# Kernel tuning notes

Hardware: AMD Instinct MI355X
Metric: run time of the kernel (lower is better)

## Reference

```python
import jax, jax.numpy as jnp
import numpy as np

B, N, C, H, P = 8, 4096, 512, 8, 64
D = C // H


def setup_inputs() -> dict:
    key = jax.random.key(0)
    ks = jax.random.split(key, 5)
    s = 0.02
    return {
        "x": jax.random.normal(ks[0], (B, N, C), jnp.float32),
        "w_qkv": jax.random.normal(ks[1], (3 * C, C), jnp.float32) * s,
        "w_e": jax.random.normal(ks[2], (P, N), jnp.float32) * s,
        "b_e": jnp.zeros((P,), jnp.float32),
        "temperature": jnp.ones((1, 1, 1), jnp.float32),
        "temperature2": jnp.ones((H, 1, 1), jnp.float32),
        "w_o1": jax.random.normal(ks[3], (C // 2, C), jnp.float32) * s,
        "b_o1": jnp.zeros((C // 2,), jnp.float32),
        "w_o2": jax.random.normal(ks[4], (C // 2, C), jnp.float32) * s,
        "b_o2": jnp.zeros((C // 2,), jnp.float32),
    }


def reference(x, w_qkv, w_e, b_e, temperature, temperature2, w_o1, b_o1, w_o2, b_o2):
    Bs, Ns, Cs = x.shape
    # qkvv projection and head split: [B,N,3C] -> [3,B,H,N,D]
    qkv = (x @ w_qkv.T).reshape(Bs, Ns, 3, H, D)
    qkv = jnp.transpose(qkv, (2, 0, 3, 1, 4))
    q, k, v = qkv[0], qkv[1], qkv[2]
    q_t = jnp.swapaxes(q, -2, -1)  # [B,H,D,N]
    k_t = jnp.swapaxes(k, -2, -1)  # [B,H,D,N]
    v_t = jnp.swapaxes(v, -2, -1)  # [B,H,D,N]
    # Linformer-style projection along token axis; E = F (shared weights)
    kp = k_t @ w_e.T + b_e  # [B,H,D,P]
    vp = v_t @ w_e.T + b_e  # [B,H,D,P]
    # L2-normalize q along tokens (k is normalized in the original AFTER
    # projection, so that normalization is dead code and omitted)
    qn = q_t / jnp.maximum(jnp.linalg.norm(q_t, axis=-1, keepdims=True), 1e-12)
    # ---- channel attention: [B,C,C] scores over raw x ----
    xt = jnp.swapaxes(x, -2, -1)  # [B,C,N]
    attn_ca = jax.nn.softmax((xt @ x) * temperature, axis=-1)
    x_ca = jnp.swapaxes(attn_ca @ xt, -2, -1)  # [B,N,C]
    # ---- projected spatial attention: [B,H,N,P] scores ----
    attn_sa = jax.nn.softmax(
        jnp.einsum('bhdn,bhdp->bhnp', qn, kp) * temperature2, axis=-1)
    x_sa = jnp.einsum('bhnp,bhdp->bhnd', attn_sa, vp)  # [B,H,N,D]
    # faithful to torch: permute(0,3,1,2) then reshape(B,N,C)
    x_sa = jnp.transpose(x_sa, (0, 3, 1, 2)).reshape(Bs, Ns, Cs)
    out = jnp.concatenate(
        [x_sa @ w_o1.T + b_o1, x_ca @ w_o2.T + b_o2], axis=-1)
    return out
```

## Files before the change

### kernel.cpp

```cpp
#include <hip/hip_runtime.h>
#include <hip/hip_bf16.h>

typedef unsigned short u16;

#define AS1 __attribute__((address_space(1)))
#define AS3 __attribute__((address_space(3)))

static __device__ __forceinline__ float bl(u16 v) {
    return __uint_as_float(((unsigned)v) << 16);
}
static __device__ __forceinline__ u16 f2b(float f) {
    unsigned u = __float_as_uint(f);
    unsigned r = u + 0x7FFFu + ((u >> 16) & 1u);
    return (u16)(r >> 16);
}
static __device__ __forceinline__ float ldf(const void* p, long i, int isbf) {
    if (isbf) return bl(((const u16*)p)[i]);
    return ((const float*)p)[i];
}
static __device__ __forceinline__ void gload_lds16(const u16* g, u16* l) {
    __builtin_amdgcn_global_load_lds((const AS1 void*)g, (AS3 void*)l, 16, 0, 0);
}

typedef __attribute__((ext_vector_type(8))) short bf16x8;
typedef __attribute__((ext_vector_type(4))) float f32x4;

static __device__ __forceinline__ bf16x8 pack8(const float* p) {
    const float4 x0 = ((const float4*)p)[0];
    const float4 x1 = ((const float4*)p)[1];
    unsigned r0, r1, r2, r3;
    asm("v_cvt_pk_bf16_f32 %0, %1, %2" : "=v"(r0) : "v"(x0.x), "v"(x0.y));
    asm("v_cvt_pk_bf16_f32 %0, %1, %2" : "=v"(r1) : "v"(x0.z), "v"(x0.w));
    asm("v_cvt_pk_bf16_f32 %0, %1, %2" : "=v"(r2) : "v"(x1.x), "v"(x1.y));
    asm("v_cvt_pk_bf16_f32 %0, %1, %2" : "=v"(r3) : "v"(x1.z), "v"(x1.w));
    union { unsigned u[4]; bf16x8 v; } u;
    u.u[0] = r0; u.u[1] = r1; u.u[2] = r2; u.u[3] = r3;
    return u.v;
}

__global__ void dtype_probe(const void* __restrict__ temp, unsigned* __restrict__ flag) {
    if (threadIdx.x == 0 && blockIdx.x == 0)
        flag[0] = (((const u16*)temp)[0] == 0x3F80) ? 1u : 0u;
}

__global__ __launch_bounds__(256) void zero_f32(float* __restrict__ p, long n) {
    const long stride = (long)gridDim.x * 256;
    for (long i = (long)blockIdx.x * 256 + threadIdx.x; i < n; i += stride)
        p[i] = 0.f;
}

__global__ __launch_bounds__(256) void conv_x(const void* __restrict__ X,
                                              u16* __restrict__ xb,
                                              u16* __restrict__ xt,
                                              const unsigned* __restrict__ flg)
{
    __shared__ u16 tile[64][65];
    const int f = (int)flg[0];
    const int b = blockIdx.z;
    const int n0 = blockIdx.x * 64, c0 = blockIdx.y * 64;
    const int t = threadIdx.x, r0 = t >> 6, c = t & 63;
    #pragma unroll
    for (int rr = 0; rr < 16; ++rr) {
        const int r = rr * 4 + r0;
        const long gi = ((long)b * 4096 + n0 + r) * 512 + c0 + c;
        const u16 h = f2b(ldf(X, gi, f));
        xb[gi] = h;
        tile[r][c] = h;
    }
    __syncthreads();
    #pragma unroll
    for (int rr = 0; rr < 16; ++rr) {
        const int cc = rr * 4 + r0;
        xt[((long)b * 512 + c0 + cc) * 4096 + n0 + c] = tile[c][cc];
    }
}

__global__ __launch_bounds__(256) void conv_w(const void* __restrict__ W,
                                              u16* __restrict__ wb, long nelem,
                                              const unsigned* __restrict__ flg)
{
    const int f = (int)flg[0];
    const long stride = (long)gridDim.x * 256;
    for (long i = (long)blockIdx.x * 256 + threadIdx.x; i < nelem; i += stride)
        wb[i] = f2b(ldf(W, i, f));
}

__global__ __launch_bounds__(512, 2) void gemm256_nt(
    const u16* __restrict__ A, const u16* __restrict__ B,
    void* __restrict__ C, const void* __restrict__ bias,
    int K, int lda, int ldb, int ldc,
    long sA, long sB, long sC,
    const unsigned* __restrict__ flg, int biasExt, int cF32,
    float* __restrict__ qsq,
    const u16* __restrict__ A2, const u16* __restrict__ B2,
    const void* __restrict__ bias2, int nSwitch)
{
    __shared__ u16 Asm[2][256 * 32];
    __shared__ u16 Bsm[2][256 * 32];
    const int t = threadIdx.x, w = t >> 6, l = t & 63;
    const int gx = gridDim.x, gy = gridDim.y;
    const long nwg = (long)gx * gy * gridDim.z;
    const long lin = blockIdx.x + (long)gx * (blockIdx.y + (long)gy * blockIdx.z);
    long nid = lin;
    if ((nwg & 7) == 0) nid = (lin & 7) * (nwg >> 3) + (lin >> 3);
    const int by = (int)(nid % gy);
    const long r2 = nid / gy;
    const int bx = (int)(r2 % gx);
    const int bz = (int)(r2 / gx);
    const int m0 = bx * 256, n0 = by * 256;
    const u16* Asel = A; const u16* Bsel = B; const void* bsel = bias;
    int nLoc = n0;
    if (A2 && n0 >= nSwitch) { Asel = A2; Bsel = B2; bsel = bias2; nLoc = n0 - nSwitch; }
    const u16* Ab = Asel + (long)bz * sA;
    const u16* Bb = Bsel + (long)bz * sB + (long)nLoc * ldb;
    const int wm = (w >> 1) * 64, wn = (w & 1) * 128;
    const int srow = l >> 2;
    const int selem = (((l & 3) ^ (srow & 3)) << 3);
    const int fr = l & 15;
    const int fk = (l >> 4) * 8;
    const int xorv = (fr & 3) << 3;
    f32x4 acc[4][8];
    #pragma unroll
    for (int i = 0; i < 4; ++i)
        #pragma unroll
        for (int j = 0; j < 8; ++j)
            acc[i][j] = (f32x4){0.f, 0.f, 0.f, 0.f};

#define STAGE256(nb, kk)                                                                     \
    do {                                                                                     \
        gload_lds16(Ab + (long)(m0 + w * 16 + srow) * lda + (kk) + selem, &Asm[nb][w * 512]);        \
        gload_lds16(Ab + (long)(m0 + (w + 8) * 16 + srow) * lda + (kk) + selem, &Asm[nb][(w + 8) * 512]); \
        gload_lds16(Bb + (long)(w * 16 + srow) * ldb + (kk) + selem, &Bsm[nb][w * 512]);             \
        gload_lds16(Bb + (long)((w + 8) * 16 + srow) * ldb + (kk) + selem, &Bsm[nb][(w + 8) * 512]);     \
    } while (0)

    STAGE256(0, 0);
    __syncthreads();
    int cur = 0;
    for (int k0 = 0; k0 < K; k0 += 32) {
        if (k0 + 32 < K) STAGE256(cur ^ 1, k0 + 32);
        bf16x8 af[4], bf[8];
        #pragma unroll
        for (int i = 0; i < 4; ++i)
            af[i] = *(const bf16x8*)&Asm[cur][((wm + i * 16 + fr) << 5) + (fk ^ xorv)];
        #pragma unroll
        for (int j = 0; j < 8; ++j)
            bf[j] = *(const bf16x8*)&Bsm[cur][((wn + j * 16 + fr) << 5) + (fk ^ xorv)];
        #pragma unroll
        for (int i = 0; i < 4; ++i)
            #pragma unroll
            for (int j = 0; j < 8; ++j)
                acc[i][j] = __builtin_amdgcn_mfma_f32_16x16x32_bf16(af[i], bf[j], acc[i][j], 0, 0, 0);
        __syncthreads();
        cur ^= 1;
    }
#undef STAGE256

    const int f = (int)flg[0];
    const long cOff = (long)bz * sC;
    float bj[8];
    #pragma unroll
    for (int j = 0; j < 8; ++j) bj[j] = 0.f;
    if (bsel) {
        #pragma unroll
        for (int j = 0; j < 8; ++j)
            bj[j] = ldf(bsel, (nLoc & 255) + wn + j * 16 + fr, biasExt ? f : 1);
    }
    #pragma unroll
    for (int i = 0; i < 4; ++i) {
        #pragma unroll
        for (int j = 0; j < 8; ++j) {
            const int col = n0 + wn + j * 16 + fr;
            #pragma unroll
            for (int r = 0; r < 4; ++r) {
                const int row = m0 + wm + i * 16 + (l >> 4) * 4 + r;
                const float v = acc[i][j][r] + bj[j];
                if (cF32) ((float*)C)[cOff + (long)row * ldc + col] = v;
                else      ((u16*)C)[cOff + (long)row * ldc + col] = f2b(v);
            }
        }
    }
    if (qsq) {
        #pragma unroll
        for (int j = 0; j < 8; ++j) {
            const int col = n0 + wn + j * 16 + fr;
            if (col < 512) {
                float s = 0.f;
                #pragma unroll
                for (int i = 0; i < 4; ++i)
                    #pragma unroll
                    for (int r = 0; r < 4; ++r)
                        s = fmaf(acc[i][j][r], acc[i][j][r], s);
                s += __shfl_xor(s, 16, 64);
                s += __shfl_xor(s, 32, 64);
                if ((l >> 4) == 0)
                    atomicAdd(&qsq[(long)bz * 512 + col], s);
            }
        }
    }
}

__global__ __launch_bounds__(512, 2) void gram256_sym(
    const u16* __restrict__ XT, float* __restrict__ S)
{
    __shared__ u16 Asm[2][256 * 32];
    __shared__ u16 Bsm[2][256 * 32];
    const int t = threadIdx.x, w = t >> 6, l = t & 63;
    const int tx = blockIdx.x, b = blockIdx.y, kz = blockIdx.z;
    const int diag = (tx != 1);
    const int m0 = (tx == 2) ? 256 : 0;
    const int n0 = (tx == 0) ? 0 : 256;
    const u16* Ab = XT + (long)b * 512 * 4096 + (long)m0 * 4096;
    const u16* Bb = XT + (long)b * 512 * 4096 + (long)n0 * 4096;
    const int wm = (w >> 1) * 64, wn = (w & 1) * 128;
    const int srow = l >> 2;
    const int selem = (((l & 3) ^ (srow & 3)) << 3);
    const int fr = l & 15;
    const int fk = (l >> 4) * 8;
    const int xorv = (fr & 3) << 3;
    f32x4 acc[4][8];
    #pragma unroll
    for (int i = 0; i < 4; ++i)
        #pragma unroll
        for (int j = 0; j < 8; ++j)
            acc[i][j] = (f32x4){0.f, 0.f, 0.f, 0.f};

#define GSTAGE(nb, kk)                                                                       \
    do {                                                                                     \
        gload_lds16(Ab + (long)(w * 16 + srow) * 4096 + (kk) + selem, &Asm[nb][w * 512]);            \
        gload_lds16(Ab + (long)((w + 8) * 16 + srow) * 4096 + (kk) + selem, &Asm[nb][(w + 8) * 512]);    \
        if (!diag) {                                                                         \
            gload_lds16(Bb + (long)(w * 16 + srow) * 4096 + (kk) + selem, &Bsm[nb][w * 512]);        \
            gload_lds16(Bb + (long)((w + 8) * 16 + srow) * 4096 + (kk) + selem, &Bsm[nb][(w + 8) * 512]); \
        }                                                                                    \
    } while (0)

    const int kBeg = kz * 1024, kEnd = kBeg + 1024;
    GSTAGE(0, kBeg);
    __syncthreads();
    int cur = 0;
    for (int k0 = kBeg; k0 < kEnd; k0 += 32) {
        if (k0 + 32 < kEnd) GSTAGE(cur ^ 1, k0 + 32);
        const u16* Bsrc = diag ? &Asm[cur][0] : &Bsm[cur][0];
        bf16x8 af[4], bf[8];
        #pragma unroll
        for (int i = 0; i < 4; ++i)
            af[i] = *(const bf16x8*)&Asm[cur][((wm + i * 16 + fr) << 5) + (fk ^ xorv)];
        #pragma unroll
        for (int j = 0; j < 8; ++j)
            bf[j] = *(const bf16x8*)&Bsrc[((wn + j * 16 + fr) << 5) + (fk ^ xorv)];
        #pragma unroll
        for (int i = 0; i < 4; ++i)
            #pragma unroll
            for (int j = 0; j < 8; ++j)
                acc[i][j] = __builtin_amdgcn_mfma_f32_16x16x32_bf16(af[i], bf[j], acc[i][j], 0, 0, 0);
        __syncthreads();
        cur ^= 1;
    }
#undef GSTAGE

    float* Sb = S + (long)b * 262144;
    #pragma unroll
    for (int i = 0; i < 4; ++i) {
        #pragma unroll
        for (int j = 0; j < 8; ++j) {
            const int col = n0 + wn + j * 16 + fr;
            #pragma unroll
            for (int r = 0; r < 4; ++r) {
                const int row = m0 + wm + i * 16 + (l >> 4) * 4 + r;
                const float v = acc[i][j][r];
                atomicAdd(&Sb[(long)row * 512 + col], v);
                if (!diag) atomicAdd(&Sb[(long)col * 512 + row], v);
            }
        }
    }
}

__global__ __launch_bounds__(256) void xe_mfma(const u16* __restrict__ WEB,
                                               const u16* __restrict__ XT,
                                               float* __restrict__ XE)
{
    const int t = threadIdx.x, w = t >> 6, l = t & 63;
    const int l15 = l & 15, g = l >> 4;
    const int c0 = blockIdx.x * 128 + (w >> 1) * 64;
    const int b = blockIdx.y;
    const int nbase = blockIdx.z * 512 + (w & 1) * 256;
    f32x4 acc[4][4];
    #pragma unroll
    for (int i = 0; i < 4; ++i)
        #pragma unroll
        for (int j = 0; j < 4; ++j)
            acc[i][j] = (f32x4){0.f, 0.f, 0.f, 0.f};
    for (int ks = 0; ks < 8; ++ks) {
        const int n = nbase + ks * 32 + g * 8;
        bf16x8 a[4], bb[4];
        #pragma unroll
        for (int i = 0; i < 4; ++i)
            a[i] = *(const bf16x8*)&WEB[(long)(i * 16 + l15) * 4096 + n];
        #pragma unroll
        for (int j = 0; j < 4; ++j)
            bb[j] = *(const bf16x8*)&XT[((long)b * 512 + c0 + j * 16 + l15) * 4096 + n];
        #pragma unroll
        for (int i = 0; i < 4; ++i)
            #pragma unroll
            for (int j = 0; j < 4; ++j)
                acc[i][j] = __builtin_amdgcn_mfma_f32_16x16x32_bf16(a[i], bb[j], acc[i][j], 0, 0, 0);
    }
    #pragma unroll
    for (int i = 0; i < 4; ++i)
        #pragma unroll
        for (int j = 0; j < 4; ++j)
            #pragma unroll
            for (int r = 0; r < 4; ++r)
                atomicAdd(&XE[((long)b * 64 + i * 16 + g * 4 + r) * 512 + c0 + j * 16 + l15],
                          acc[i][j][r]);
}

__global__ __launch_bounds__(256) void kpvp2_mfma(const float* __restrict__ XE,
                                                  const u16* __restrict__ WQB,
                                                  const float* __restrict__ qsq,
                                                  const void* __restrict__ be,
                                                  const void* __restrict__ temp2,
                                                  u16* __restrict__ kpT,
                                                  u16* __restrict__ vpB,
                                                  const unsigned* __restrict__ flg)
{
    __shared__ float lds[4][4096];
    const int bh = blockIdx.x, b = bh >> 3, h = bh & 7;
    const int t = threadIdx.x, w = t >> 6, l = t & 63;
    const int l15 = l & 15, g = l >> 4;
    const int isV = w >> 1;
    const int ch = w & 1;
    const u16* wrow = WQB + (long)(512 + isV * 512 + h * 64) * 512;
    const float* xr = XE + (long)b * 64 * 512;
    f32x4 acc[4][4];
    #pragma unroll
    for (int i = 0; i < 4; ++i)
        #pragma unroll
        for (int j = 0; j < 4; ++j)
            acc[i][j] = (f32x4){0.f, 0.f, 0.f, 0.f};
    for (int ks = 0; ks < 8; ++ks) {
        const int c = ch * 256 + ks * 32 + g * 8;
        bf16x8 a[4], bb[4];
        if (!isV) {
            #pragma unroll
            for (int i = 0; i < 4; ++i)
                a[i] = pack8(&xr[(long)(i * 16 + l15) * 512 + c]);
            #pragma unroll
            for (int j = 0; j < 4; ++j)
                bb[j] = *(const bf16x8*)&wrow[(long)(j * 16 + l15) * 512 + c];
        } else {
            #pragma unroll
            for (int i = 0; i < 4; ++i)
                a[i] = *(const bf16x8*)&wrow[(long)(i * 16 + l15) * 512 + c];
            #pragma unroll
            for (int j = 0; j < 4; ++j)
                bb[j] = pack8(&xr[(long)(j * 16 + l15) * 512 + c]);
        }
        #pragma unroll
        for (int i = 0; i < 4; ++i)
            #pragma unroll
            for (int j = 0; j < 4; ++j)
                acc[i][j] = __builtin_amdgcn_mfma_f32_16x16x32_bf16(a[i], bb[j], acc[i][j], 0, 0, 0);
    }
    #pragma unroll
    for (int i = 0; i < 4; ++i)
        #pragma unroll
        for (int j = 0; j < 4; ++j)
            #pragma unroll
            for (int r = 0; r < 4; ++r)
                lds[w][(i * 16 + g * 4 + r) * 64 + j * 16 + l15] = acc[i][j][r];
    __syncthreads();
    const int f = (int)flg[0];
    if (t < 128) {
        const float t2 = ldf(temp2, h, f);
        for (int e = t; e < 4096; e += 128) {
            const int p = e >> 6, d = e & 63;
            const float rn = 1.0f / fmaxf(sqrtf(qsq[b * 512 + h * 64 + d]), 1e-12f);
            kpT[(long)bh * 4096 + e] = f2b((lds[0][e] + lds[1][e] + ldf(be, p, f)) * rn * t2);
        }
    } else {
        for (int e = t - 128; e < 4096; e += 128) {
            vpB[(long)bh * 4096 + e] = f2b(lds[2][e] + lds[3][e] + ldf(be, e & 63, f));
        }
    }
}

__global__ __launch_bounds__(256) void softmax_ca(const float* __restrict__ S,
                                                  u16* __restrict__ A,
                                                  const void* __restrict__ temp,
                                                  const unsigned* __restrict__ flg)
{
    __shared__ float red[256];
    const int row = blockIdx.x;
    const int t = threadIdx.x;
    const float tv = ldf(temp, 0, (int)flg[0]);
    const float* s = S + (long)row * 512;
    float v0 = s[t] * tv;
    float v1 = s[t + 256] * tv;
    red[t] = fmaxf(v0, v1);
    __syncthreads();
    for (int o = 128; o > 0; o >>= 1) {
        if (t < o) red[t] = fmaxf(red[t], red[t + o]);
        __syncthreads();
    }
    const float m = red[0];
    __syncthreads();
    float e0 = expf(v0 - m), e1 = expf(v1 - m);
    red[t] = e0 + e1;
    __syncthreads();
    for (int o = 128; o > 0; o >>= 1) {
        if (t < o) red[t] += red[t + o];
        __syncthreads();
    }
    const float inv = 1.0f / red[0];
    u16* a = A + (long)row * 512;
    a[t]       = f2b(e0 * inv);
    a[t + 256] = f2b(e1 * inv);
}

__global__ __launch_bounds__(256) void spatial_attn_mfma(
    const u16* __restrict__ Q, const u16* __restrict__ kpT,
    const u16* __restrict__ vpB, u16* __restrict__ XSA)
{
    __shared__ u16 P[4][4096];
    const int bh = blockIdx.y, b = bh >> 3, h = bh & 7;
    const int t = threadIdx.x, w = t >> 6, l = t & 63;
    const int l15 = l & 15, g = l >> 4;
    const int n0 = blockIdx.x * 256 + w * 64;
    char* Pw = (char*)&P[w][0];

    const u16* kb = kpT + (long)bh * 4096;
    const u16* vb = vpB + (long)bh * 4096;
    bf16x8 akp[2][4], avp[2][4];
    #pragma unroll
    for (int ks = 0; ks < 2; ++ks)
        #pragma unroll
        for (int i = 0; i < 4; ++i) {
            akp[ks][i] = *(const bf16x8*)&kb[(i * 16 + l15) * 64 + ks * 32 + g * 8];
            avp[ks][i] = *(const bf16x8*)&vb[(i * 16 + l15) * 64 + ks * 32 + g * 8];
        }

    f32x4 sacc[4][4];
    #pragma unroll
    for (int i = 0; i < 4; ++i)
        #pragma unroll
        for (int j = 0; j < 4; ++j)
            sacc[i][j] = (f32x4){0.f, 0.f, 0.f, 0.f};
    const u16* qb = Q + ((long)b * 4096 + n0) * 512 + h * 64;
    #pragma unroll
    for (int ks = 0; ks < 2; ++ks) {
        bf16x8 bq[4];
        #pragma unroll
        for (int j = 0; j < 4; ++j)
            bq[j] = *(const bf16x8*)&qb[(long)(j * 16 + l15) * 512 + ks * 32 + g * 8];
        #pragma unroll
        for (int i = 0; i < 4; ++i)
            #pragma unroll
            for (int j = 0; j < 4; ++j)
                sacc[i][j] = __builtin_amdgcn_mfma_f32_16x16x32_bf16(akp[ks][i], bq[j], sacc[i][j], 0, 0, 0);
    }

    #pragma unroll
    for (int j = 0; j < 4; ++j) {
        float m = sacc[0][j][0];
        #pragma unroll
        for (int i = 0; i < 4; ++i)
            #pragma unroll
            for (int r = 0; r < 4; ++r)
                m = fmaxf(m, sacc[i][j][r]);
        m = fmaxf(m, __shfl_xor(m, 16, 64));
        m = fmaxf(m, __shfl_xor(m, 32, 64));
        float s = 0.f;
        #pragma unroll
        for (int i = 0; i < 4; ++i)
            #pragma unroll
            for (int r = 0; r < 4; ++r) {
                const float e = __expf(sacc[i][j][r] - m);
                sacc[i][j][r] = e;
                s += e;
            }
        s += __shfl_xor(s, 16, 64);
        s += __shfl_xor(s, 32, 64);
        const float inv = 1.0f / s;
        const int n = j * 16 + l15;
        const int swz = (n & 7) << 4;
        #pragma unroll
        for (int i = 0; i < 4; ++i) {
            unsigned lo, hi;
            float p0 = sacc[i][j][0] * inv, p1 = sacc[i][j][1] * inv;
            float p2 = sacc[i][j][2] * inv, p3 = sacc[i][j][3] * inv;
            asm("v_cvt_pk_bf16_f32 %0, %1, %2" : "=v"(lo) : "v"(p0), "v"(p1));
            asm("v_cvt_pk_bf16_f32 %0, %1, %2" : "=v"(hi) : "v"(p2), "v"(p3));
            const int byte = (n * 128 + i * 32 + g * 8) ^ swz;
            *(uint2*)(Pw + byte) = make_uint2(lo, hi);
        }
    }

    f32x4 oacc[4][4];
    #pragma unroll
    for (int i = 0; i < 4; ++i)
        #pragma unroll
        for (int j = 0; j < 4; ++j)
            oacc[i][j] = (f32x4){0.f, 0.f, 0.f, 0.f};
    #pragma unroll
    for (int ks = 0; ks < 2; ++ks) {
        bf16x8 bp[4];
        #pragma unroll
        for (int j = 0; j < 4; ++j) {
            const int n = j * 16 + l15;
            const int byte = (n * 128 + ks * 64 + g * 16) ^ ((n & 7) << 4);
            bp[j] = *(const bf16x8*)(Pw + byte);
        }
        #pragma unroll
        for (int i = 0; i < 4; ++i)
            #pragma unroll
            for (int j = 0; j < 4; ++j)
                oacc[i][j] = __builtin_amdgcn_mfma_f32_16x16x32_bf16(avp[ks][i], bp[j], oacc[i][j], 0, 0, 0);
    }

    const int rowoff = h * 8 + (n0 >> 9);
    const int colbase = n0 & 511;
    #pragma unroll
    for (int i = 0; i < 4; ++i)
        #pragma unroll
        for (int r = 0; r < 4; ++r) {
            const int d = i * 16 + g * 4 + r;
            u16* orow = XSA + ((long)b * 4096 + d * 64 + rowoff) * 512 + colbase;
            #pragma unroll
            for (int j = 0; j < 4; ++j)
                orow[j * 16 + l15] = f2b(oacc[i][j][r]);
        }
}

extern "C" void kernel_launch(void* const* d_in, const int* in_sizes, int n_in,
                              void* d_out, int out_size, void* d_ws, size_t ws_size,
                              hipStream_t stream)
{
    const void* x     = d_in[0];
    const void* w_qkv = d_in[1];
    const void* w_e   = d_in[2];
    const void* b_e   = d_in[3];
    const void* temp  = d_in[4];
    const void* temp2 = d_in[5];
    const void* w_o1  = d_in[6];
    const void* b_o1  = d_in[7];
    const void* w_o2  = d_in[8];
    const void* b_o2  = d_in[9];
    float* out = (float*)d_out;

    char* ws = (char*)d_ws;
    unsigned* flag = (unsigned*)ws; ws += 256;
    u16*   qb     = (u16*)ws;   ws += (size_t)8 * 4096 * 512 * 2;
    float* qsq    = (float*)ws; ws += (size_t)4096 * 4;
    float* xe     = (float*)ws; ws += (size_t)8 * 64 * 512 * 4;
    float* scores = (float*)ws; ws += (size_t)8 * 512 * 512 * 4;
    u16*   attn   = (u16*)ws;   ws += (size_t)8 * 512 * 512 * 2;
    u16*   x_ca   = (u16*)ws;   ws += (size_t)8 * 4096 * 512 * 2;
    u16*   xt     = (u16*)ws;   ws += (size_t)8 * 512 * 4096 * 2;
    u16*   xb     = (u16*)ws;   ws += (size_t)8 * 4096 * 512 * 2;
    u16*   wqb    = (u16*)ws;   ws += (size_t)1536 * 512 * 2;
    u16*   web    = (u16*)ws;   ws += (size_t)64 * 4096 * 2;
    u16*   wo1b   = (u16*)ws;   ws += (size_t)256 * 512 * 2;
    u16*   wo2b   = (u16*)ws;   ws += (size_t)256 * 512 * 2;
    u16*   kpT    = (u16*)ws;   ws += (size_t)262144 * 2;
    u16*   vpB    = (u16*)ws;   ws += (size_t)262144 * 2;
    u16*   x_sa   = xt;

    dtype_probe<<<1, 64, 0, stream>>>(temp, flag);
    conv_x<<<dim3(64, 8, 8), 256, 0, stream>>>(x, xb, xt, flag);
    conv_w<<<768, 256, 0, stream>>>(w_qkv, wqb, 1536L * 512, flag);
    conv_w<<<128, 256, 0, stream>>>(w_e, web, 64L * 4096, flag);
    conv_w<<<128, 256, 0, stream>>>(w_o1, wo1b, 256L * 512, flag);
    conv_w<<<128, 256, 0, stream>>>(w_o2, wo2b, 256L * 512, flag);
    zero_f32<<<4, 256, 0, stream>>>(qsq, 4096);
    gemm256_nt<<<dim3(16, 2, 8), 512, 0, stream>>>(
        xb, wqb, qb, nullptr, 512, 512, 512, 512,
        (long)4096 * 512, 0, (long)4096 * 512, flag, 0, 0, qsq,
        nullptr, nullptr, nullptr, 1 << 30);
    zero_f32<<<128, 256, 0, stream>>>(xe, (long)8 * 64 * 512);
    xe_mfma<<<dim3(4, 8, 8), 256, 0, stream>>>(web, xt, xe);
    kpvp2_mfma<<<64, 256, 0, stream>>>(xe, wqb, qsq, b_e, temp2, kpT, vpB, flag);
    zero_f32<<<2048, 256, 0, stream>>>(scores, (long)8 * 512 * 512);
    gram256_sym<<<dim3(3, 8, 4), 512, 0, stream>>>(xt, scores);
    softmax_ca<<<4096, 256, 0, stream>>>(scores, attn, temp, flag);
    gemm256_nt<<<dim3(16, 2, 8), 512, 0, stream>>>(
        xb, attn, x_ca, nullptr, 512, 512, 512, 512,
        (long)4096 * 512, (long)512 * 512, (long)4096 * 512, flag, 0, 0, nullptr,
        nullptr, nullptr, nullptr, 1 << 30);
    spatial_attn_mfma<<<dim3(16, 64), 256, 0, stream>>>(qb, kpT, vpB, x_sa);
    gemm256_nt<<<dim3(16, 2, 8), 512, 0, stream>>>(
        x_sa, wo1b, out, b_o1, 512, 512, 512, 512,
        (long)4096 * 512, 0, (long)4096 * 512, flag, 1, 1, nullptr,
        x_ca, wo2b, b_o2, 256);
}
```

Before: 417.3 us.

## Replace atomic gram split-K with 128-tile partial buffers summed in softmax

The channel-attention Gram kernel moves from 256x256 tiles (3 upper-triangular blocks per batch) to 128x128 tiles (10 upper-triangular blocks) with 256-thread blocks. Each split-K slice now writes plain stores into its own partial-score buffer instead of atomically adding into one shared buffer, so the zero-fill kernel is dropped. The softmax kernel sums the four partials when it reads each row. This aims to remove atomic traffic and the memset and to launch more blocks, at the cost of four times the score workspace, extra reads in softmax, and dropping the XOR LDS swizzle, which may bring back bank conflicts.

```diff
diff --git a/kernel.cpp b/kernel.cpp
--- a/kernel.cpp
+++ b/kernel.cpp
@@ -200,39 +200,43 @@
     }
 }
 
-__global__ __launch_bounds__(512, 2) void gram256_sym(
-    const u16* __restrict__ XT, float* __restrict__ S)
-{
-    __shared__ u16 Asm[2][256 * 32];
-    __shared__ u16 Bsm[2][256 * 32];
+__global__ __launch_bounds__(256) void gram128_sym(
+    const u16* __restrict__ XT, float* __restrict__ SP)
+{
+    __shared__ u16 Asm[2][128 * 32];
+    __shared__ u16 Bsm[2][128 * 32];
     const int t = threadIdx.x, w = t >> 6, l = t & 63;
     const int tx = blockIdx.x, b = blockIdx.y, kz = blockIdx.z;
-    const int diag = (tx != 1);
-    const int m0 = (tx == 2) ? 256 : 0;
-    const int n0 = (tx == 0) ? 0 : 256;
+    int ti, tj;
+    if (tx < 4)      { ti = 0; tj = tx; }
+    else if (tx < 7) { ti = 1; tj = tx - 3; }
+    else if (tx < 9) { ti = 2; tj = tx - 5; }
+    else             { ti = 3; tj = 3; }
+    const int diag = (ti == tj);
+    const int m0 = ti * 128, n0 = tj * 128;
     const u16* Ab = XT + (long)b * 512 * 4096 + (long)m0 * 4096;
     const u16* Bb = XT + (long)b * 512 * 4096 + (long)n0 * 4096;
-    const int wm = (w >> 1) * 64, wn = (w & 1) * 128;
+    const int wm = (w >> 1) * 64, wn = (w & 1) * 64;
     const int srow = l >> 2;
-    const int selem = (((l & 3) ^ (srow & 3)) << 3);
+    const int scol = (l & 3) * 8;
     const int fr = l & 15;
     const int fk = (l >> 4) * 8;
-    const int xorv = (fr & 3) << 3;
-    f32x4 acc[4][8];
-    #pragma unroll
-    for (int i = 0; i < 4; ++i)
-        #pragma unroll
-        for (int j = 0; j < 8; ++j)
+    f32x4 acc[4][4];
+    #pragma unroll
+    for (int i = 0; i < 4; ++i)
+        #pragma unroll
+        for (int j = 0; j < 4; ++j)
             acc[i][j] = (f32x4){0.f, 0.f, 0.f, 0.f};
 
-#define GSTAGE(nb, kk)                                                                       \
-    do {                                                                                     \
-        gload_lds16(Ab + (long)(w * 16 + srow) * 4096 + (kk) + selem, &Asm[nb][w * 512]);            \
-        gload_lds16(Ab + (long)((w + 8) * 16 + srow) * 4096 + (kk) + selem, &Asm[nb][(w + 8) * 512]);    \
-        if (!diag) {                                                                         \
-            gload_lds16(Bb + (long)(w * 16 + srow) * 4096 + (kk) + selem, &Bsm[nb][w * 512]);        \
-            gload_lds16(Bb + (long)((w + 8) * 16 + srow) * 4096 + (kk) + selem, &Bsm[nb][(w + 8) * 512]); \
-        }                                                                                    \
+    const int q0 = w, q1 = w + 4;
+#define GSTAGE(nb, kk)                                                                  \
+    do {                                                                                \
+        gload_lds16(Ab + (long)(q0 * 16 + srow) * 4096 + (kk) + scol, &Asm[nb][q0 * 512]);      \
+        gload_lds16(Ab + (long)(q1 * 16 + srow) * 4096 + (kk) + scol, &Asm[nb][q1 * 512]);      \
+        if (!diag) {                                                                    \
+            gload_lds16(Bb + (long)(q0 * 16 + srow) * 4096 + (kk) + scol, &Bsm[nb][q0 * 512]);  \
+            gload_lds16(Bb + (long)(q1 * 16 + srow) * 4096 + (kk) + scol, &Bsm[nb][q1 * 512]);  \
+        }                                                                               \
     } while (0)
 
     const int kBeg = kz * 1024, kEnd = kBeg + 1024;
@@ -242,35 +246,34 @@
     for (int k0 = kBeg; k0 < kEnd; k0 += 32) {
         if (k0 + 32 < kEnd) GSTAGE(cur ^ 1, k0 + 32);
         const u16* Bsrc = diag ? &Asm[cur][0] : &Bsm[cur][0];
-        bf16x8 af[4], bf[8];
-        #pragma unroll
-        for (int i = 0; i < 4; ++i)
-            af[i] = *(const bf16x8*)&Asm[cur][((wm + i * 16 + fr) << 5) + (fk ^ xorv)];
-        #pragma unroll
-        for (int j = 0; j < 8; ++j)
-            bf[j] = *(const bf16x8*)&Bsrc[((wn + j * 16 + fr) << 5) + (fk ^ xorv)];
-        #pragma unroll
-        for (int i = 0; i < 4; ++i)
-            #pragma unroll
-            for (int j = 0; j < 8; ++j)
+        bf16x8 af[4], bf[4];
+        #pragma unroll
+        for (int i = 0; i < 4; ++i) {
+            af[i] = *(const bf16x8*)&Asm[cur][(wm + i * 16 + fr) * 32 + fk];
+            bf[i] = *(const bf16x8*)&Bsrc[(wn + i * 16 + fr) * 32 + fk];
+        }
+        #pragma unroll
+        for (int i = 0; i < 4; ++i)
+            #pragma unroll
+            for (int j = 0; j < 4; ++j)
                 acc[i][j] = __builtin_amdgcn_mfma_f32_16x16x32_bf16(af[i], bf[j], acc[i][j], 0, 0, 0);
         __syncthreads();
         cur ^= 1;
     }
 #undef GSTAGE
 
-    float* Sb = S + (long)b * 262144;
+    float* Sb = SP + ((long)kz * 8 + b) * 262144;
     #pragma unroll
     for (int i = 0; i < 4; ++i) {
         #pragma unroll
-        for (int j = 0; j < 8; ++j) {
+        for (int j = 0; j < 4; ++j) {
             const int col = n0 + wn + j * 16 + fr;
             #pragma unroll
             for (int r = 0; r < 4; ++r) {
                 const int row = m0 + wm + i * 16 + (l >> 4) * 4 + r;
                 const float v = acc[i][j][r];
-                atomicAdd(&Sb[(long)row * 512 + col], v);
-                if (!diag) atomicAdd(&Sb[(long)col * 512 + row], v);
+                Sb[(long)row * 512 + col] = v;
+                if (!diag) Sb[(long)col * 512 + row] = v;
             }
         }
     }
@@ -386,7 +389,7 @@
     }
 }
 
-__global__ __launch_bounds__(256) void softmax_ca(const float* __restrict__ S,
+__global__ __launch_bounds__(256) void softmax_ca(const float* __restrict__ SP,
                                                   u16* __restrict__ A,
                                                   const void* __restrict__ temp,
                                                   const unsigned* __restrict__ flg)
@@ -395,9 +398,12 @@
     const int row = blockIdx.x;
     const int t = threadIdx.x;
     const float tv = ldf(temp, 0, (int)flg[0]);
-    const float* s = S + (long)row * 512;
-    float v0 = s[t] * tv;
-    float v1 = s[t + 256] * tv;
+    const float* s = SP + (long)row * 512;
+    const long kzs = (long)8 * 512 * 512;
+    float v0 = s[t] + s[kzs + t] + s[2 * kzs + t] + s[3 * kzs + t];
+    float v1 = s[t + 256] + s[kzs + t + 256] + s[2 * kzs + t + 256] + s[3 * kzs + t + 256];
+    v0 *= tv;
+    v1 *= tv;
     red[t] = fmaxf(v0, v1);
     __syncthreads();
     for (int o = 128; o > 0; o >>= 1) {
@@ -554,7 +560,7 @@
     u16*   qb     = (u16*)ws;   ws += (size_t)8 * 4096 * 512 * 2;
     float* qsq    = (float*)ws; ws += (size_t)4096 * 4;
     float* xe     = (float*)ws; ws += (size_t)8 * 64 * 512 * 4;
-    float* scores = (float*)ws; ws += (size_t)8 * 512 * 512 * 4;
+    float* scpart = (float*)ws; ws += (size_t)4 * 8 * 512 * 512 * 4;
     u16*   attn   = (u16*)ws;   ws += (size_t)8 * 512 * 512 * 2;
     u16*   x_ca   = (u16*)ws;   ws += (size_t)8 * 4096 * 512 * 2;
     u16*   xt     = (u16*)ws;   ws += (size_t)8 * 512 * 4096 * 2;
@@ -581,9 +587,8 @@
     zero_f32<<<128, 256, 0, stream>>>(xe, (long)8 * 64 * 512);
     xe_mfma<<<dim3(4, 8, 8), 256, 0, stream>>>(web, xt, xe);
     kpvp2_mfma<<<64, 256, 0, stream>>>(xe, wqb, qsq, b_e, temp2, kpT, vpB, flag);
-    zero_f32<<<2048, 256, 0, stream>>>(scores, (long)8 * 512 * 512);
-    gram256_sym<<<dim3(3, 8, 4), 512, 0, stream>>>(xt, scores);
-    softmax_ca<<<4096, 256, 0, stream>>>(scores, attn, temp, flag);
+    gram128_sym<<<dim3(10, 8, 4), 256, 0, stream>>>(xt, scpart);
+    softmax_ca<<<4096, 256, 0, stream>>>(scpart, attn, temp, flag);
     gemm256_nt<<<dim3(16, 2, 8), 512, 0, stream>>>(
         xb, attn, x_ca, nullptr, 512, 512, 512, 512,
         (long)4096 * 512, (long)512 * 512, (long)4096 * 512, flag, 0, 0, nullptr,
```

Result: faster. 374.4 us (-10.3%).
